# Optimization experiments

Measured on AMD Instinct MI355X. Metric: run time of the kernel, lower is better.

## Reference

```python
import jax, jax.numpy as jnp
import numpy as np

D_MODEL = 768
N_HEADS = 12


def setup_inputs() -> dict:
    key = jax.random.key(0)
    ks = jax.random.split(key, 9)
    s = 1.0 / np.sqrt(D_MODEL)
    return {
        "x": jax.random.normal(ks[0], (1, 4096, D_MODEL), dtype=jnp.float32),
        "w_q": jax.random.normal(ks[1], (D_MODEL, D_MODEL), dtype=jnp.float32) * s,
        "b_q": jnp.zeros((D_MODEL,), dtype=jnp.float32),
        "w_k": jax.random.normal(ks[2], (D_MODEL, D_MODEL), dtype=jnp.float32) * s,
        "b_k": jnp.zeros((D_MODEL,), dtype=jnp.float32),
        "w_v": jax.random.normal(ks[3], (D_MODEL, D_MODEL), dtype=jnp.float32) * s,
        "b_v": jnp.zeros((D_MODEL,), dtype=jnp.float32),
        "w_o": jax.random.normal(ks[4], (D_MODEL, D_MODEL), dtype=jnp.float32) * s,
        "b_o": jnp.zeros((D_MODEL,), dtype=jnp.float32),
    }


def reference(x, w_q, b_q, w_k, b_k, w_v, b_v, w_o, b_o):
    b, l, dm = x.shape
    h = N_HEADS
    dk = dm // h
    # projections ([b,l,dm] @ [dm,dm]) then split heads -> [b,h,l,dk]
    def proj(w, bias):
        y = x @ w + bias
        return y.reshape(b, l, h, dk).transpose(0, 2, 1, 3)
    q = proj(w_q, b_q)
    k = proj(w_k, b_k)
    v = proj(w_v, b_v)
    scale = jnp.asarray(dk, x.dtype) ** 0.5
    scores = jnp.einsum("bhqd,bhkd->bhqk", q, k)  # [b,h,l,l]
    causal = jnp.triu(jnp.ones((l, l), dtype=bool), k=1)
    scores = jnp.where(causal, -jnp.inf, scores)
    weights = jax.nn.softmax(scores / scale, axis=-1)
    heads = jnp.einsum("bhqk,bhkd->bhqd", weights, v)  # [b,h,l,dk]
    heads = heads.transpose(0, 2, 1, 3).reshape(b, l, dm)
    return heads @ w_o + b_o
```

## Files before the change

### kernel.cpp

```cpp
#include <hip/hip_runtime.h>

#define L_SEQ 4096
#define DMODEL 768
#define NH 12
#define DK 64

typedef __bf16 bf16;
typedef __bf16 bf16x8 __attribute__((ext_vector_type(8)));
typedef __bf16 bf16x4 __attribute__((ext_vector_type(4)));
typedef float f32x4 __attribute__((ext_vector_type(4)));

#define QSCALE 0.1803368801111204f
#define DEFER_THR 8.0f

__device__ __forceinline__ void gload16(const void* g, void* l) {
    __builtin_amdgcn_global_load_lds(
        (const __attribute__((address_space(1))) unsigned int*)g,
        (__attribute__((address_space(3))) unsigned int*)l, 16, 0, 0);
}

__global__ __launch_bounds__(256) void prep_kernel(
    const float* __restrict__ x,
    const float* __restrict__ w_q, const float* __restrict__ w_k,
    const float* __restrict__ w_v, const float* __restrict__ w_o,
    bf16* __restrict__ xb, bf16* __restrict__ wqt, bf16* __restrict__ wkt,
    bf16* __restrict__ wvt, bf16* __restrict__ wot)
{
    const int bid = blockIdx.x;
    const int t = threadIdx.x;
    if (bid < 576) {
        __shared__ bf16 Ls[64][72];
        const int mat = bid / 144;
        const int tile = bid % 144;
        const int k0 = (tile / 12) * 64;
        const int c0 = (tile % 12) * 64;
        const float* W = mat == 0 ? w_q : mat == 1 ? w_k : mat == 2 ? w_v : w_o;
        bf16* WT = mat == 0 ? wqt : mat == 1 ? wkt : mat == 2 ? wvt : wot;
        #pragma unroll
        for (int p = 0; p < 4; ++p) {
            int id = t + p * 256;
            int r = id >> 4, c4 = id & 15;
            float4 v = *(const float4*)(W + (size_t)(k0 + r) * DMODEL + c0 + c4 * 4);
            bf16x4 b; b[0] = (bf16)v.x; b[1] = (bf16)v.y; b[2] = (bf16)v.z; b[3] = (bf16)v.w;
            *(bf16x4*)&Ls[r][c4 * 4] = b;
        }
        __syncthreads();
        #pragma unroll
        for (int p = 0; p < 2; ++p) {
            int id = t + p * 256;
            int crow = id >> 3, kc = id & 7;
            bf16x8 o;
            #pragma unroll
            for (int e = 0; e < 8; ++e) o[e] = Ls[kc * 8 + e][crow];
            *(bf16x8*)(WT + (size_t)(c0 + crow) * DMODEL + k0 + kc * 8) = o;
        }
    } else {
        const size_t base = (size_t)(bid - 576) * 4096;
        #pragma unroll
        for (int p = 0; p < 4; ++p) {
            size_t idx = base + (size_t)(t + p * 256) * 4;
            float4 v = *(const float4*)(x + idx);
            bf16x4 b; b[0] = (bf16)v.x; b[1] = (bf16)v.y; b[2] = (bf16)v.z; b[3] = (bf16)v.w;
            *(bf16x4*)(xb + idx) = b;
        }
    }
}

__global__ __launch_bounds__(256) void proj_kernel(
    const bf16* __restrict__ xb,
    const bf16* __restrict__ wqt, const bf16* __restrict__ wkt, const bf16* __restrict__ wvt,
    const float* __restrict__ b_q, const float* __restrict__ b_k, const float* __restrict__ b_v,
    bf16* __restrict__ qbuf, bf16* __restrict__ kbuf, bf16* __restrict__ vt)
{
    __shared__ bf16 As[128][72];
    __shared__ bf16 Bs[64][72];
    const int t = threadIdx.x;
    const int w = t >> 6, l = t & 63;
    const int lg = l >> 4, lr = l & 15;

    if (blockIdx.x < 768) {
        const int bn = blockIdx.x % 24;
        const int bm = blockIdx.x / 24;
        const int m0 = bm * 128;
        const int gn0 = bn * 64;
        const int sel = gn0 / DMODEL;
        const int c0 = gn0 % DMODEL;
        const bf16* WT = sel ? wkt : wqt;
        const float* bias = sel ? b_k : b_q;
        const float scale = sel ? 1.0f : QSCALE;

        f32x4 acc[2][4];
        #pragma unroll
        for (int i = 0; i < 2; i++)
            #pragma unroll
            for (int j = 0; j < 4; j++) acc[i][j] = (f32x4){0.f, 0.f, 0.f, 0.f};

        for (int kk = 0; kk < DMODEL; kk += 64) {
            #pragma unroll
            for (int p = 0; p < 4; ++p) {
                int id = t + p * 256;
                int row = id >> 3, ch = id & 7;
                *(bf16x8*)&As[row][ch * 8] =
                    *(const bf16x8*)(xb + (size_t)(m0 + row) * DMODEL + kk + ch * 8);
            }
            #pragma unroll
            for (int p = 0; p < 2; ++p) {
                int id = t + p * 256;
                int n = id >> 3, ch = id & 7;
                *(bf16x8*)&Bs[n][ch * 8] =
                    *(const bf16x8*)(WT + (size_t)(c0 + n) * DMODEL + kk + ch * 8);
            }
            __syncthreads();
            #pragma unroll
            for (int ks = 0; ks < 2; ++ks) {
                bf16x8 a[2], bfr[4];
                #pragma unroll
                for (int i = 0; i < 2; i++) a[i] = *(const bf16x8*)&As[w * 32 + i * 16 + lr][ks * 32 + lg * 8];
                #pragma unroll
                for (int j = 0; j < 4; j++) bfr[j] = *(const bf16x8*)&Bs[j * 16 + lr][ks * 32 + lg * 8];
                #pragma unroll
                for (int i = 0; i < 2; i++)
                    #pragma unroll
                    for (int j = 0; j < 4; j++)
                        acc[i][j] = __builtin_amdgcn_mfma_f32_16x16x32_bf16(a[i], bfr[j], acc[i][j], 0, 0, 0);
            }
            __syncthreads();
        }
        #pragma unroll
        for (int i = 0; i < 2; i++) {
            #pragma unroll
            for (int j = 0; j < 4; j++) {
                int c = c0 + j * 16 + lr;
                int h = c >> 6, d = c & 63;
                float bb = bias[c];
                #pragma unroll
                for (int r = 0; r < 4; r++) {
                    int m = m0 + w * 32 + i * 16 + lg * 4 + r;
                    float v = (acc[i][j][r] + bb) * scale;
                    if (sel == 0) {
                        qbuf[((size_t)h * L_SEQ + m) * DK + d] = (bf16)v;
                    } else {
                        size_t idx = (size_t)h * L_SEQ * DK + (size_t)(m >> 6) * 4096
                                   + (size_t)(m & 63) * 64 + (((d >> 3) ^ (m & 7)) << 3) + (d & 7);
                        kbuf[idx] = (bf16)v;
                    }
                }
            }
        }
    } else {
        const int bid = blockIdx.x - 768;
        const int bc = bid % 12;
        const int bmm = bid / 12;
        const int c0 = bc * 64;
        const int mm0 = bmm * 128;

        f32x4 acc[8];
        #pragma unroll
        for (int j = 0; j < 8; j++) acc[j] = (f32x4){0.f, 0.f, 0.f, 0.f};

        for (int kk = 0; kk < DMODEL; kk += 64) {
            #pragma unroll
            for (int p = 0; p < 4; ++p) {
                int id = t + p * 256;
                int row = id >> 3, ch = id & 7;
                *(bf16x8*)&As[row][ch * 8] =
                    *(const bf16x8*)(xb + (size_t)(mm0 + row) * DMODEL + kk + ch * 8);
            }
            #pragma unroll
            for (int p = 0; p < 2; ++p) {
                int id = t + p * 256;
                int n = id >> 3, ch = id & 7;
                *(bf16x8*)&Bs[n][ch * 8] =
                    *(const bf16x8*)(wvt + (size_t)(c0 + n) * DMODEL + kk + ch * 8);
            }
            __syncthreads();
            #pragma unroll
            for (int ks = 0; ks < 2; ++ks) {
                bf16x8 a = *(const bf16x8*)&Bs[w * 16 + lr][ks * 32 + lg * 8];
                #pragma unroll
                for (int j = 0; j < 8; j++) {
                    bf16x8 b = *(const bf16x8*)&As[j * 16 + lr][ks * 32 + lg * 8];
                    acc[j] = __builtin_amdgcn_mfma_f32_16x16x32_bf16(a, b, acc[j], 0, 0, 0);
                }
            }
            __syncthreads();
        }
        #pragma unroll
        for (int j = 0; j < 8; j++) {
            int m = mm0 + j * 16 + lr;
            #pragma unroll
            for (int r = 0; r < 4; r++) {
                int c = c0 + w * 16 + lg * 4 + r;
                float v = acc[j][r] + b_v[c];
                size_t idx = (size_t)(c >> 6) * DK * L_SEQ + (size_t)(m >> 6) * 4096
                           + (size_t)(c & 63) * 64 + ((((m >> 3) & 7) ^ (c & 7)) << 3) + (m & 7);
                vt[idx] = (bf16)v;
            }
        }
    }
}

__global__ __launch_bounds__(512) void attn_kernel(
    const bf16* __restrict__ qbuf, const bf16* __restrict__ kbuf,
    const bf16* __restrict__ vt, bf16* __restrict__ obuf)
{
    __shared__ __align__(16) char lds[65536];

    const int bid = blockIdx.x;
    const int h  = bid % NH;
    const int qt = 63 - (bid / NH);
    const int q0 = qt * 64;
    const int nt = qt + 1;
    const int nit = (nt + 1) >> 1;

    const int t = threadIdx.x;
    const int w = t >> 6;
    const int g = w >> 2;
    const int wg = w & 3;
    const int l = t & 63;
    const int lg = l >> 4, lr = l & 15;
    const int tg = t & 255;
    const int sw = (lr & 7) << 4;

    float* mergeAcc = (float*)lds;
    float* mergeM   = (float*)(lds + 22528);

    const size_t qrow = (size_t)h * L_SEQ + q0 + wg * 16 + lr;
    const bf16x8 qa0 = *(const bf16x8*)(qbuf + qrow * DK + 0  + lg * 8);
    const bf16x8 qa1 = *(const bf16x8*)(qbuf + qrow * DK + 32 + lg * 8);

    bf16x8 ones;
    #pragma unroll
    for (int e = 0; e < 8; ++e) ones[e] = (bf16)1.0f;

    f32x4 acc[4];
    #pragma unroll
    for (int j = 0; j < 4; j++) acc[j] = (f32x4){0.f, 0.f, 0.f, 0.f};
    f32x4 acc_sum = (f32x4){0.f, 0.f, 0.f, 0.f};
    float run_m = -1e30f;

    const bf16* kb_base = kbuf + (size_t)h * L_SEQ * DK;
    const bf16* vt_base = vt + (size_t)h * DK * L_SEQ;

    if (g < nt) {
        const bf16* kg = kb_base + (size_t)g * 4096;
        const bf16* vg = vt_base + (size_t)g * 4096;
        char* kl = lds + (size_t)(g << 1) * 8192;
        char* vl = lds + 32768 + (size_t)(g << 1) * 8192;
        #pragma unroll
        for (int p = 0; p < 2; ++p) {
            int id = tg + p * 256;
            gload16(kg + id * 8, kl + id * 16);
            gload16(vg + id * 8, vl + id * 16);
        }
    }

    for (int it = 0; it < nit; ++it) {
        const int cur = 2 * it + g;
        const bool active = (cur < nt);
        const int b = it & 1;
        asm volatile("s_waitcnt vmcnt(0)" ::: "memory");
        __builtin_amdgcn_sched_barrier(0);
        __builtin_amdgcn_s_barrier();
        const int nxt = cur + 2;
        if (nxt < nt) {
            const bf16* kg = kb_base + (size_t)nxt * 4096;
            const bf16* vg = vt_base + (size_t)nxt * 4096;
            char* kl = lds + (size_t)((g << 1) | (b ^ 1)) * 8192;
            char* vl = lds + 32768 + (size_t)((g << 1) | (b ^ 1)) * 8192;
            #pragma unroll
            for (int p = 0; p < 2; ++p) {
                int id = tg + p * 256;
                gload16(kg + id * 8, kl + id * 16);
                gload16(vg + id * 8, vl + id * 16);
            }
        }
        if (active) {
            char* Kbase = lds + (size_t)((g << 1) | b) * 8192;
            char* Vbase = lds + 32768 + (size_t)((g << 1) | b) * 8192;
            f32x4 s[4];
            #pragma unroll
            for (int j = 0; j < 4; j++) s[j] = (f32x4){0.f, 0.f, 0.f, 0.f};
            __builtin_amdgcn_s_setprio(1);
            #pragma unroll
            for (int dh = 0; dh < 2; ++dh) {
                const bf16x8 qa = dh ? qa1 : qa0;
                #pragma unroll
                for (int j = 0; j < 4; j++) {
                    bf16x8 kb = *(const bf16x8*)(Kbase + (j * 16 + lr) * 128 + ((dh * 64 + lg * 16) ^ sw));
                    s[j] = __builtin_amdgcn_mfma_f32_16x16x32_bf16(kb, qa, s[j], 0, 0, 0);
                }
            }
            __builtin_amdgcn_s_setprio(0);
            if (cur == qt) {
                const int qoff = wg * 16 + lr;
                #pragma unroll
                for (int j = 0; j < 4; j++)
                    #pragma unroll
                    for (int r = 0; r < 4; r++)
                        if (j * 16 + lg * 4 + r > qoff) s[j][r] = -3e30f;
            }
            float m0 = fmaxf(fmaxf(s[0][0], s[0][1]), s[0][2]);
            float m1 = fmaxf(fmaxf(s[0][3], s[1][0]), s[1][1]);
            float m2 = fmaxf(fmaxf(s[1][2], s[1][3]), s[2][0]);
            float m3 = fmaxf(fmaxf(s[2][1], s[2][2]), s[2][3]);
            float m4 = fmaxf(fmaxf(s[3][0], s[3][1]), s[3][2]);
            float t1 = fmaxf(fmaxf(m0, m1), m2);
            float t2 = fmaxf(fmaxf(m3, m4), s[3][3]);
            float mx = fmaxf(t1, t2);
            mx = fmaxf(mx, __shfl_xor(mx, 16));
            mx = fmaxf(mx, __shfl_xor(mx, 32));
            if (!__all(mx <= run_m + DEFER_THR)) {
                const float nm = fmaxf(run_m, mx);
                const float scq = exp2f(run_m - nm);
                run_m = nm;
                float sc0 = __shfl(scq, lg * 4 + 0);
                float sc1 = __shfl(scq, lg * 4 + 1);
                float sc2 = __shfl(scq, lg * 4 + 2);
                float sc3 = __shfl(scq, lg * 4 + 3);
                #pragma unroll
                for (int jd = 0; jd < 4; jd++) {
                    acc[jd][0] *= sc0; acc[jd][1] *= sc1;
                    acc[jd][2] *= sc2; acc[jd][3] *= sc3;
                }
                acc_sum[0] *= sc0; acc_sum[1] *= sc1;
                acc_sum[2] *= sc2; acc_sum[3] *= sc3;
            }
            unsigned Wp[4][2];
            #pragma unroll
            for (int j = 0; j < 4; j++) {
                float e0 = exp2f(s[j][0] - run_m);
                float e1 = exp2f(s[j][1] - run_m);
                float e2 = exp2f(s[j][2] - run_m);
                float e3 = exp2f(s[j][3] - run_m);
                asm("v_cvt_pk_bf16_f32 %0, %1, %2" : "=v"(Wp[j][0]) : "v"(e0), "v"(e1));
                asm("v_cvt_pk_bf16_f32 %0, %1, %2" : "=v"(Wp[j][1]) : "v"(e2), "v"(e3));
            }
            __builtin_amdgcn_s_setprio(1);
            #pragma unroll
            for (int dh = 0; dh < 2; ++dh) {
                unsigned x0 = Wp[2 * dh][0], y0 = Wp[2 * dh + 1][0];
                unsigned x1 = Wp[2 * dh][1], y1 = Wp[2 * dh + 1][1];
                asm("v_permlane32_swap_b32 %0, %1" : "+v"(x0), "+v"(y0));
                asm("v_permlane16_swap_b32 %0, %1" : "+v"(x0), "+v"(y0));
                asm("v_permlane32_swap_b32 %0, %1" : "+v"(x1), "+v"(y1));
                asm("v_permlane16_swap_b32 %0, %1" : "+v"(x1), "+v"(y1));
                union { unsigned u[4]; bf16x8 v; } pk;
                pk.u[0] = x0; pk.u[1] = x1; pk.u[2] = y0; pk.u[3] = y1;
                const bf16x8 pa = pk.v;
                acc_sum = __builtin_amdgcn_mfma_f32_16x16x32_bf16(pa, ones, acc_sum, 0, 0, 0);
                #pragma unroll
                for (int jd = 0; jd < 4; jd++) {
                    bf16x8 vb = *(const bf16x8*)(Vbase + (jd * 16 + lr) * 128 + ((dh * 64 + lg * 16) ^ sw));
                    acc[jd] = __builtin_amdgcn_mfma_f32_16x16x32_bf16(pa, vb, acc[jd], 0, 0, 0);
                }
            }
            __builtin_amdgcn_s_setprio(0);
        }
    }

    __syncthreads();
    if (g == 1) {
        float* base = mergeAcc + (size_t)(wg * 64 + l) * 21;
        #pragma unroll
        for (int jd = 0; jd < 4; jd++)
            #pragma unroll
            for (int r = 0; r < 4; r++) base[jd * 4 + r] = acc[jd][r];
        #pragma unroll
        for (int r = 0; r < 4; r++) base[16 + r] = acc_sum[r];
        mergeM[wg * 64 + l] = run_m;
    }
    __syncthreads();
    if (g == 0) {
        const float* base = mergeAcc + (size_t)(wg * 64 + l) * 21;
        const float mB = mergeM[wg * 64 + l];
        const float mF = fmaxf(run_m, mB);
        const float sa = exp2f(run_m - mF);
        const float sb = exp2f(mB - mF);
        float a4[4], b4[4];
        #pragma unroll
        for (int r = 0; r < 4; r++) {
            a4[r] = __shfl(sa, lg * 4 + r);
            b4[r] = __shfl(sb, lg * 4 + r);
        }
        #pragma unroll
        for (int jd = 0; jd < 4; jd++) {
            #pragma unroll
            for (int r = 0; r < 4; r++) {
                float denom = acc_sum[r] * a4[r] + base[16 + r] * b4[r];
                float v = acc[jd][r] * a4[r] + base[jd * 4 + r] * b4[r];
                int m = q0 + wg * 16 + lg * 4 + r;
                obuf[(size_t)m * DMODEL + h * DK + jd * 16 + lr] = (bf16)(v / denom);
            }
        }
    }
}

__global__ __launch_bounds__(256) void out_proj_kernel(
    const bf16* __restrict__ obuf, const bf16* __restrict__ wot,
    const float* __restrict__ b_o, float* __restrict__ out)
{
    __shared__ bf16 As[128][72];
    __shared__ bf16 Bts[64][72];
    const int bn = blockIdx.x % 12;
    const int bm = blockIdx.x / 12;
    const int m0 = bm * 128, c0 = bn * 64;
    const int t = threadIdx.x;
    const int w = t >> 6, l = t & 63, lg = l >> 4, lr = l & 15;

    f32x4 acc[2][4];
    #pragma unroll
    for (int i = 0; i < 2; i++)
        #pragma unroll
        for (int j = 0; j < 4; j++) acc[i][j] = (f32x4){0.f, 0.f, 0.f, 0.f};

    for (int kk = 0; kk < DMODEL; kk += 64) {
        #pragma unroll
        for (int p = 0; p < 4; ++p) {
            int id = t + p * 256;
            int row = id >> 3, ch = id & 7;
            *(bf16x8*)&As[row][ch * 8] =
                *(const bf16x8*)(obuf + (size_t)(m0 + row) * DMODEL + kk + ch * 8);
        }
        #pragma unroll
        for (int p = 0; p < 2; ++p) {
            int id = t + p * 256;
            int n = id >> 3, ch = id & 7;
            *(bf16x8*)&Bts[n][ch * 8] =
                *(const bf16x8*)(wot + (size_t)(c0 + n) * DMODEL + kk + ch * 8);
        }
        __syncthreads();
        #pragma unroll
        for (int ks = 0; ks < 2; ++ks) {
            bf16x8 a[2], bfr[4];
            #pragma unroll
            for (int i = 0; i < 2; i++) a[i] = *(const bf16x8*)&As[w * 32 + i * 16 + lr][ks * 32 + lg * 8];
            #pragma unroll
            for (int j = 0; j < 4; j++) bfr[j] = *(const bf16x8*)&Bts[j * 16 + lr][ks * 32 + lg * 8];
            #pragma unroll
            for (int i = 0; i < 2; i++)
                #pragma unroll
                for (int j = 0; j < 4; j++)
                    acc[i][j] = __builtin_amdgcn_mfma_f32_16x16x32_bf16(a[i], bfr[j], acc[i][j], 0, 0, 0);
        }
        __syncthreads();
    }
    #pragma unroll
    for (int i = 0; i < 2; i++) {
        #pragma unroll
        for (int j = 0; j < 4; j++) {
            int c = c0 + j * 16 + lr;
            float bb = b_o[c];
            #pragma unroll
            for (int r = 0; r < 4; r++) {
                int m = m0 + w * 32 + i * 16 + lg * 4 + r;
                out[(size_t)m * DMODEL + c] = acc[i][j][r] + bb;
            }
        }
    }
}

extern "C" void kernel_launch(void* const* d_in, const int* in_sizes, int n_in,
                              void* d_out, int out_size, void* d_ws, size_t ws_size,
                              hipStream_t stream) {
    const float* x   = (const float*)d_in[0];
    const float* w_q = (const float*)d_in[1];
    const float* b_q = (const float*)d_in[2];
    const float* w_k = (const float*)d_in[3];
    const float* b_k = (const float*)d_in[4];
    const float* w_v = (const float*)d_in[5];
    const float* b_v = (const float*)d_in[6];
    const float* w_o = (const float*)d_in[7];
    const float* b_o = (const float*)d_in[8];
    float* out = (float*)d_out;

    char* ws = (char*)d_ws;
    const size_t SZ = (size_t)NH * L_SEQ * DK * sizeof(bf16);
    const size_t WTSZ = (size_t)DMODEL * DMODEL * sizeof(bf16);
    bf16* qbuf = (bf16*)(ws);
    bf16* kbuf = (bf16*)(ws + SZ);
    bf16* vt   = (bf16*)(ws + 2 * SZ);
    bf16* obuf = (bf16*)(ws + 3 * SZ);
    bf16* xb   = (bf16*)(ws + 4 * SZ);
    bf16* wqt  = (bf16*)(ws + 5 * SZ);
    bf16* wkt  = (bf16*)(ws + 5 * SZ + WTSZ);
    bf16* wvt  = (bf16*)(ws + 5 * SZ + 2 * WTSZ);
    bf16* wot  = (bf16*)(ws + 5 * SZ + 3 * WTSZ);

    prep_kernel<<<dim3(1344), dim3(256), 0, stream>>>(x, w_q, w_k, w_v, w_o, xb, wqt, wkt, wvt, wot);
    proj_kernel<<<dim3(1152), dim3(256), 0, stream>>>(xb, wqt, wkt, wvt, b_q, b_k, b_v, qbuf, kbuf, vt);
    attn_kernel<<<dim3(768), dim3(512), 0, stream>>>(qbuf, kbuf, vt, obuf);
    out_proj_kernel<<<dim3(384), dim3(256), 0, stream>>>(obuf, wot, b_o, out);
}
```

Measured before the change: 115.3 us.

## Software-pipeline QK^T one tile ahead with triple-buffered K and register-staged V

Restructures the attention main loop so the QK^T MFMAs for the next KV tile are issued before the softmax and PV of the current tile. K now uses a three-deep LDS ring filled with async global-to-LDS loads. V is loaded into registers and written to a single LDS buffer after an extra barrier. It also adds a minimum-blocks hint of 4 to launch_bounds. The aim is to hide softmax latency behind matrix work and overlap loads, at the cost of more registers, an extra barrier per iteration and possible occupancy pressure.

```diff
diff --git a/kernel.cpp b/kernel.cpp
--- a/kernel.cpp
+++ b/kernel.cpp
@@ -200,7 +200,7 @@
     }
 }
 
-__global__ __launch_bounds__(512) void attn_kernel(
+__global__ __launch_bounds__(512, 4) void attn_kernel(
     const bf16* __restrict__ qbuf, const bf16* __restrict__ kbuf,
     const bf16* __restrict__ vt, bf16* __restrict__ obuf)
 {
@@ -224,6 +224,8 @@
 
     float* mergeAcc = (float*)lds;
     float* mergeM   = (float*)(lds + 22528);
+    char* const Kb = lds + (size_t)g * 24576;
+    char* const Vb = lds + 49152 + (size_t)g * 8192;
 
     const size_t qrow = (size_t)h * L_SEQ + q0 + wg * 16 + lr;
     const bf16x8 qa0 = *(const bf16x8*)(qbuf + qrow * DK + 0  + lg * 8);
@@ -242,71 +244,92 @@
     const bf16* kb_base = kbuf + (size_t)h * L_SEQ * DK;
     const bf16* vt_base = vt + (size_t)h * DK * L_SEQ;
 
+    bf16x8 vreg0, vreg1;
     if (g < nt) {
         const bf16* kg = kb_base + (size_t)g * 4096;
         const bf16* vg = vt_base + (size_t)g * 4096;
-        char* kl = lds + (size_t)(g << 1) * 8192;
-        char* vl = lds + 32768 + (size_t)(g << 1) * 8192;
-        #pragma unroll
-        for (int p = 0; p < 2; ++p) {
-            int id = tg + p * 256;
-            gload16(kg + id * 8, kl + id * 16);
-            gload16(vg + id * 8, vl + id * 16);
+        gload16(kg + tg * 8, Kb + tg * 16);
+        gload16(kg + (tg + 256) * 8, Kb + (tg + 256) * 16);
+        vreg0 = *(const bf16x8*)(vg + tg * 8);
+        vreg1 = *(const bf16x8*)(vg + (tg + 256) * 8);
+    }
+    if (g + 2 < nt) {
+        const bf16* kg = kb_base + (size_t)(g + 2) * 4096;
+        gload16(kg + tg * 8, Kb + 8192 + tg * 16);
+        gload16(kg + (tg + 256) * 8, Kb + 8192 + (tg + 256) * 16);
+    }
+    asm volatile("s_waitcnt vmcnt(0)" ::: "memory");
+    __builtin_amdgcn_sched_barrier(0);
+    __builtin_amdgcn_s_barrier();
+
+    f32x4 S[4];
+    #pragma unroll
+    for (int j = 0; j < 4; j++) S[j] = (f32x4){0.f, 0.f, 0.f, 0.f};
+    if (g < nt) {
+        *(bf16x8*)(Vb + tg * 16) = vreg0;
+        *(bf16x8*)(Vb + (tg + 256) * 16) = vreg1;
+        #pragma unroll
+        for (int dh = 0; dh < 2; ++dh) {
+            const bf16x8 qa = dh ? qa1 : qa0;
+            #pragma unroll
+            for (int j = 0; j < 4; j++) {
+                bf16x8 kv = *(const bf16x8*)(Kb + (j * 16 + lr) * 128 + ((dh * 64 + lg * 16) ^ sw));
+                S[j] = __builtin_amdgcn_mfma_f32_16x16x32_bf16(kv, qa, S[j], 0, 0, 0);
+            }
         }
     }
 
     for (int it = 0; it < nit; ++it) {
         const int cur = 2 * it + g;
         const bool active = (cur < nt);
-        const int b = it & 1;
-        asm volatile("s_waitcnt vmcnt(0)" ::: "memory");
+        const int nxt = cur + 2, nx2 = cur + 4;
+        asm volatile("s_waitcnt vmcnt(0) lgkmcnt(0)" ::: "memory");
         __builtin_amdgcn_sched_barrier(0);
         __builtin_amdgcn_s_barrier();
-        const int nxt = cur + 2;
         if (nxt < nt) {
-            const bf16* kg = kb_base + (size_t)nxt * 4096;
             const bf16* vg = vt_base + (size_t)nxt * 4096;
-            char* kl = lds + (size_t)((g << 1) | (b ^ 1)) * 8192;
-            char* vl = lds + 32768 + (size_t)((g << 1) | (b ^ 1)) * 8192;
-            #pragma unroll
-            for (int p = 0; p < 2; ++p) {
-                int id = tg + p * 256;
-                gload16(kg + id * 8, kl + id * 16);
-                gload16(vg + id * 8, vl + id * 16);
-            }
-        }
-        if (active) {
-            char* Kbase = lds + (size_t)((g << 1) | b) * 8192;
-            char* Vbase = lds + 32768 + (size_t)((g << 1) | b) * 8192;
-            f32x4 s[4];
-            #pragma unroll
-            for (int j = 0; j < 4; j++) s[j] = (f32x4){0.f, 0.f, 0.f, 0.f};
+            vreg0 = *(const bf16x8*)(vg + tg * 8);
+            vreg1 = *(const bf16x8*)(vg + (tg + 256) * 8);
+        }
+        if (nx2 < nt) {
+            const bf16* kg = kb_base + (size_t)nx2 * 4096;
+            char* kl = Kb + (size_t)((it + 2) % 3) * 8192;
+            gload16(kg + tg * 8, kl + tg * 16);
+            gload16(kg + (tg + 256) * 8, kl + (tg + 256) * 16);
+        }
+        f32x4 Sn[4];
+        #pragma unroll
+        for (int j = 0; j < 4; j++) Sn[j] = (f32x4){0.f, 0.f, 0.f, 0.f};
+        if (nxt < nt) {
+            char* kn = Kb + (size_t)((it + 1) % 3) * 8192;
             __builtin_amdgcn_s_setprio(1);
             #pragma unroll
             for (int dh = 0; dh < 2; ++dh) {
                 const bf16x8 qa = dh ? qa1 : qa0;
                 #pragma unroll
                 for (int j = 0; j < 4; j++) {
-                    bf16x8 kb = *(const bf16x8*)(Kbase + (j * 16 + lr) * 128 + ((dh * 64 + lg * 16) ^ sw));
-                    s[j] = __builtin_amdgcn_mfma_f32_16x16x32_bf16(kb, qa, s[j], 0, 0, 0);
+                    bf16x8 kv = *(const bf16x8*)(kn + (j * 16 + lr) * 128 + ((dh * 64 + lg * 16) ^ sw));
+                    Sn[j] = __builtin_amdgcn_mfma_f32_16x16x32_bf16(kv, qa, Sn[j], 0, 0, 0);
                 }
             }
             __builtin_amdgcn_s_setprio(0);
+        }
+        if (active) {
             if (cur == qt) {
                 const int qoff = wg * 16 + lr;
                 #pragma unroll
                 for (int j = 0; j < 4; j++)
                     #pragma unroll
                     for (int r = 0; r < 4; r++)
-                        if (j * 16 + lg * 4 + r > qoff) s[j][r] = -3e30f;
-            }
-            float m0 = fmaxf(fmaxf(s[0][0], s[0][1]), s[0][2]);
-            float m1 = fmaxf(fmaxf(s[0][3], s[1][0]), s[1][1]);
-            float m2 = fmaxf(fmaxf(s[1][2], s[1][3]), s[2][0]);
-            float m3 = fmaxf(fmaxf(s[2][1], s[2][2]), s[2][3]);
-            float m4 = fmaxf(fmaxf(s[3][0], s[3][1]), s[3][2]);
+                        if (j * 16 + lg * 4 + r > qoff) S[j][r] = -3e30f;
+            }
+            float m0 = fmaxf(fmaxf(S[0][0], S[0][1]), S[0][2]);
+            float m1 = fmaxf(fmaxf(S[0][3], S[1][0]), S[1][1]);
+            float m2 = fmaxf(fmaxf(S[1][2], S[1][3]), S[2][0]);
+            float m3 = fmaxf(fmaxf(S[2][1], S[2][2]), S[2][3]);
+            float m4 = fmaxf(fmaxf(S[3][0], S[3][1]), S[3][2]);
             float t1 = fmaxf(fmaxf(m0, m1), m2);
-            float t2 = fmaxf(fmaxf(m3, m4), s[3][3]);
+            float t2 = fmaxf(fmaxf(m3, m4), S[3][3]);
             float mx = fmaxf(t1, t2);
             mx = fmaxf(mx, __shfl_xor(mx, 16));
             mx = fmaxf(mx, __shfl_xor(mx, 32));
@@ -329,10 +352,10 @@
             unsigned Wp[4][2];
             #pragma unroll
             for (int j = 0; j < 4; j++) {
-                float e0 = exp2f(s[j][0] - run_m);
-                float e1 = exp2f(s[j][1] - run_m);
-                float e2 = exp2f(s[j][2] - run_m);
-                float e3 = exp2f(s[j][3] - run_m);
+                float e0 = exp2f(S[j][0] - run_m);
+                float e1 = exp2f(S[j][1] - run_m);
+                float e2 = exp2f(S[j][2] - run_m);
+                float e3 = exp2f(S[j][3] - run_m);
                 asm("v_cvt_pk_bf16_f32 %0, %1, %2" : "=v"(Wp[j][0]) : "v"(e0), "v"(e1));
                 asm("v_cvt_pk_bf16_f32 %0, %1, %2" : "=v"(Wp[j][1]) : "v"(e2), "v"(e3));
             }
@@ -351,12 +374,19 @@
                 acc_sum = __builtin_amdgcn_mfma_f32_16x16x32_bf16(pa, ones, acc_sum, 0, 0, 0);
                 #pragma unroll
                 for (int jd = 0; jd < 4; jd++) {
-                    bf16x8 vb = *(const bf16x8*)(Vbase + (jd * 16 + lr) * 128 + ((dh * 64 + lg * 16) ^ sw));
+                    bf16x8 vb = *(const bf16x8*)(Vb + (jd * 16 + lr) * 128 + ((dh * 64 + lg * 16) ^ sw));
                     acc[jd] = __builtin_amdgcn_mfma_f32_16x16x32_bf16(pa, vb, acc[jd], 0, 0, 0);
                 }
             }
             __builtin_amdgcn_s_setprio(0);
         }
+        __builtin_amdgcn_s_barrier();
+        if (nxt < nt) {
+            *(bf16x8*)(Vb + tg * 16) = vreg0;
+            *(bf16x8*)(Vb + (tg + 256) * 16) = vreg1;
+        }
+        #pragma unroll
+        for (int j = 0; j < 4; j++) S[j] = Sn[j];
     }
 
     __syncthreads();
```

Result: slower. 120.2 us (+4.2%).

## Stage V tiles through registers to single-buffer V in LDS

Applied to the files above, without the earlier changes.

V tiles are now prefetched into registers with ordinary global loads rather than async global-to-LDS copies. Each iteration they are written into one V buffer per group, which shrinks shared memory from 64KB to 48KB and could let more blocks fit per CU. The cost is an extra barrier and LDS wait in the middle of each iteration before the PV MFMAs, plus more registers held for the prefetched V. V load latency must also now be covered by the QK compute phase.

```diff
diff --git a/kernel.cpp b/kernel.cpp
--- a/kernel.cpp
+++ b/kernel.cpp
@@ -204,7 +204,7 @@
     const bf16* __restrict__ qbuf, const bf16* __restrict__ kbuf,
     const bf16* __restrict__ vt, bf16* __restrict__ obuf)
 {
-    __shared__ __align__(16) char lds[65536];
+    __shared__ __align__(16) char lds[49152];
 
     const int bid = blockIdx.x;
     const int h  = bid % NH;
@@ -224,6 +224,7 @@
 
     float* mergeAcc = (float*)lds;
     float* mergeM   = (float*)(lds + 22528);
+    char* const Vb  = lds + 32768 + (size_t)g * 8192;
 
     const size_t qrow = (size_t)h * L_SEQ + q0 + wg * 16 + lr;
     const bf16x8 qa0 = *(const bf16x8*)(qbuf + qrow * DK + 0  + lg * 8);
@@ -242,43 +243,42 @@
     const bf16* kb_base = kbuf + (size_t)h * L_SEQ * DK;
     const bf16* vt_base = vt + (size_t)h * DK * L_SEQ;
 
+    bf16x8 vreg0, vreg1;
     if (g < nt) {
         const bf16* kg = kb_base + (size_t)g * 4096;
         const bf16* vg = vt_base + (size_t)g * 4096;
         char* kl = lds + (size_t)(g << 1) * 8192;
-        char* vl = lds + 32768 + (size_t)(g << 1) * 8192;
-        #pragma unroll
-        for (int p = 0; p < 2; ++p) {
-            int id = tg + p * 256;
-            gload16(kg + id * 8, kl + id * 16);
-            gload16(vg + id * 8, vl + id * 16);
-        }
+        gload16(kg + tg * 8, kl + tg * 16);
+        gload16(kg + (tg + 256) * 8, kl + (tg + 256) * 16);
+        vreg0 = *(const bf16x8*)(vg + tg * 8);
+        vreg1 = *(const bf16x8*)(vg + (tg + 256) * 8);
     }
 
     for (int it = 0; it < nit; ++it) {
         const int cur = 2 * it + g;
         const bool active = (cur < nt);
         const int b = it & 1;
-        asm volatile("s_waitcnt vmcnt(0)" ::: "memory");
+        asm volatile("s_waitcnt vmcnt(0) lgkmcnt(0)" ::: "memory");
         __builtin_amdgcn_sched_barrier(0);
         __builtin_amdgcn_s_barrier();
+        if (active) {
+            *(bf16x8*)(Vb + tg * 16) = vreg0;
+            *(bf16x8*)(Vb + (tg + 256) * 16) = vreg1;
+        }
         const int nxt = cur + 2;
         if (nxt < nt) {
             const bf16* kg = kb_base + (size_t)nxt * 4096;
             const bf16* vg = vt_base + (size_t)nxt * 4096;
             char* kl = lds + (size_t)((g << 1) | (b ^ 1)) * 8192;
-            char* vl = lds + 32768 + (size_t)((g << 1) | (b ^ 1)) * 8192;
-            #pragma unroll
-            for (int p = 0; p < 2; ++p) {
-                int id = tg + p * 256;
-                gload16(kg + id * 8, kl + id * 16);
-                gload16(vg + id * 8, vl + id * 16);
-            }
-        }
+            gload16(kg + tg * 8, kl + tg * 16);
+            gload16(kg + (tg + 256) * 8, kl + (tg + 256) * 16);
+            vreg0 = *(const bf16x8*)(vg + tg * 8);
+            vreg1 = *(const bf16x8*)(vg + (tg + 256) * 8);
+        }
+        f32x4 s[4];
+        unsigned Wp[4][2];
         if (active) {
             char* Kbase = lds + (size_t)((g << 1) | b) * 8192;
-            char* Vbase = lds + 32768 + (size_t)((g << 1) | b) * 8192;
-            f32x4 s[4];
             #pragma unroll
             for (int j = 0; j < 4; j++) s[j] = (f32x4){0.f, 0.f, 0.f, 0.f};
             __builtin_amdgcn_s_setprio(1);
@@ -326,7 +326,6 @@
                 acc_sum[0] *= sc0; acc_sum[1] *= sc1;
                 acc_sum[2] *= sc2; acc_sum[3] *= sc3;
             }
-            unsigned Wp[4][2];
             #pragma unroll
             for (int j = 0; j < 4; j++) {
                 float e0 = exp2f(s[j][0] - run_m);
@@ -336,6 +335,11 @@
                 asm("v_cvt_pk_bf16_f32 %0, %1, %2" : "=v"(Wp[j][0]) : "v"(e0), "v"(e1));
                 asm("v_cvt_pk_bf16_f32 %0, %1, %2" : "=v"(Wp[j][1]) : "v"(e2), "v"(e3));
             }
+        }
+        asm volatile("s_waitcnt lgkmcnt(0)" ::: "memory");
+        __builtin_amdgcn_sched_barrier(0);
+        __builtin_amdgcn_s_barrier();
+        if (active) {
             __builtin_amdgcn_s_setprio(1);
             #pragma unroll
             for (int dh = 0; dh < 2; ++dh) {
@@ -351,7 +355,7 @@
                 acc_sum = __builtin_amdgcn_mfma_f32_16x16x32_bf16(pa, ones, acc_sum, 0, 0, 0);
                 #pragma unroll
                 for (int jd = 0; jd < 4; jd++) {
-                    bf16x8 vb = *(const bf16x8*)(Vbase + (jd * 16 + lr) * 128 + ((dh * 64 + lg * 16) ^ sw));
+                    bf16x8 vb = *(const bf16x8*)(Vb + (jd * 16 + lr) * 128 + ((dh * 64 + lg * 16) ^ sw));
                     acc[jd] = __builtin_amdgcn_mfma_f32_16x16x32_bf16(pa, vb, acc[jd], 0, 0, 0);
                 }
             }
```

Result: no change. 116.4 us (+0.9%).
